# Kernel tuning notes

Hardware: AMD Instinct MI355X
Metric: run time of the kernel (lower is better)

The kernel has to match this reference:

```python
import jax, jax.numpy as jnp
import numpy as np

N = 100000   # nodes
E = 1200000  # edges
D = 64       # feature / hidden dim (heads=1)
L = 3        # num_layers
G = 64       # num graphs
SCALE = 1.0 / np.sqrt(D)


def setup_inputs() -> dict:
    key = jax.random.key(0)
    ks = jax.random.split(key, 12)
    inp = {
        "x": jax.random.normal(ks[0], (N, D), dtype=jnp.float32),
        "edge_index": jax.random.randint(ks[1], (2, E), 0, N, dtype=jnp.int64),
        "batch": jnp.sort(jax.random.randint(ks[2], (N,), 0, G, dtype=jnp.int64)),
        "Wq": jax.random.normal(ks[3], (L, D, D), dtype=jnp.float32) * 0.1,
        "bq": jax.random.normal(ks[4], (L, D), dtype=jnp.float32) * 0.1,
        "Wk": jax.random.normal(ks[5], (L, D, D), dtype=jnp.float32) * 0.1,
        "bk": jax.random.normal(ks[6], (L, D), dtype=jnp.float32) * 0.1,
        "Wv": jax.random.normal(ks[7], (L, D, D), dtype=jnp.float32) * 0.1,
        "bv": jax.random.normal(ks[8], (L, D), dtype=jnp.float32) * 0.1,
        "Ws": jax.random.normal(ks[9], (L, D, D), dtype=jnp.float32) * 0.1,
        "bs": jax.random.normal(ks[10], (L, D), dtype=jnp.float32) * 0.1,
    }
    return inp


def _transformer_conv(x, src, dst, Wq, bq, Wk, bk, Wv, bv, Ws, bs):
    # PyG TransformerConv, heads=1, concat=True, root_weight=True, beta=False
    q = x @ Wq + bq            # [N, D] query of target nodes
    k = x @ Wk + bk            # [N, D] key of source nodes
    v = x @ Wv + bv            # [N, D] value of source nodes
    logits = jnp.sum(q[dst] * k[src], axis=-1) * SCALE  # [E]
    # segment softmax over incoming edges of each target node
    m = jax.ops.segment_max(logits, dst, num_segments=N)        # [N]
    e = jnp.exp(logits - m[dst])                                 # [E]
    denom = jax.ops.segment_sum(e, dst, num_segments=N)         # [N]
    alpha = e / denom[dst]                                       # [E]
    agg = jax.ops.segment_sum(alpha[:, None] * v[src], dst, num_segments=N)  # [N, D]
    return agg + x @ Ws + bs   # root/skip connection


def reference(x, edge_index, batch, Wq, bq, Wk, bk, Wv, bv, Ws, bs):
    src, dst = edge_index[0], edge_index[1]
    for l in range(L):
        x = _transformer_conv(x, src, dst, Wq[l], bq[l], Wk[l], bk[l],
                              Wv[l], bv[l], Ws[l], bs[l])
        x = jax.nn.relu(x)
    # global_mean_pool
    sums = jax.ops.segment_sum(x, batch, num_segments=G)                  # [G, D]
    counts = jax.ops.segment_sum(jnp.ones((N,), x.dtype), batch, num_segments=G)
    graph_emb = sums / jnp.maximum(counts, 1.0)[:, None]
    return (x, graph_emb)
```

## Files before the change

kernel.cpp:

```cpp
#include <hip/hip_runtime.h>
#include <math.h>

#define DD 64

typedef _Float16 h2 __attribute__((ext_vector_type(2)));
typedef _Float16 h4 __attribute__((ext_vector_type(4)));
typedef _Float16 h8 __attribute__((ext_vector_type(8)));
typedef float f32x4 __attribute__((ext_vector_type(4)));

__global__ __launch_bounds__(64) void k_wconv(
    const float* __restrict__ Wq, const float* __restrict__ Wk,
    const float* __restrict__ Wv, const float* __restrict__ Ws,
    _Float16* __restrict__ wf)
{
  int bid = blockIdx.x;
  int layer = bid >> 5;
  int c = (bid >> 1) & 15;
  int s = bid & 1;
  int lane = threadIdx.x;
  int col = c * 16 + (lane & 15);
  int mi = col >> 6;
  const float* W = (mi == 0 ? Wq : mi == 1 ? Wk : mi == 2 ? Wv : Ws)
                   + (size_t)layer * DD * DD;
  int colw = col & 63;
  _Float16* o = wf + ((((size_t)(layer * 16 + c)) * 2 + s) * 64 + lane) * 8;
  #pragma unroll
  for (int j = 0; j < 8; ++j) {
    int k = s * 32 + (lane >> 4) * 8 + j;
    o[j] = (_Float16)W[k * DD + colw];
  }
}

__global__ __launch_bounds__(256) void k_xconv(
    const float* __restrict__ x, _Float16* __restrict__ xb, int total8)
{
  int i = blockIdx.x * 256 + threadIdx.x;
  if (i >= total8) return;
  float4 a = ((const float4*)x)[i * 2];
  float4 b = ((const float4*)x)[i * 2 + 1];
  h8 o;
  o[0] = (_Float16)a.x; o[1] = (_Float16)a.y; o[2] = (_Float16)a.z; o[3] = (_Float16)a.w;
  o[4] = (_Float16)b.x; o[5] = (_Float16)b.y; o[6] = (_Float16)b.z; o[7] = (_Float16)b.w;
  *(h8*)(xb + (size_t)i * 8) = o;
}

#define LH_STRIDE 200
#define LF_STRIDE 68
#define WAVE_LDS  (16 * 400 + 16 * 272)

__global__ __launch_bounds__(256) void k_projM(
    const _Float16* __restrict__ xb, const _Float16* __restrict__ wf,
    const float* __restrict__ bq, const float* __restrict__ bk,
    const float* __restrict__ bv, const float* __restrict__ bs,
    _Float16* __restrict__ qh, _Float16* __restrict__ kvh,
    float* __restrict__ sout, int n)
{
  __shared__ __align__(16) char lds[4 * WAVE_LDS];
  int wave = threadIdx.x >> 6;
  int lane = threadIdx.x & 63;
  int nbase = blockIdx.x * 64 + wave * 16;
  if (nbase >= n) return;

  char* wbase = lds + wave * WAVE_LDS;
  _Float16* lh = (_Float16*)wbase;
  float*    lf = (float*)(wbase + 16 * 400);

  const int cl = lane & 15;
  const int rq = lane >> 4;

  int ar = min(nbase + cl, n - 1);
  h8 a0 = *(const h8*)(xb + (size_t)ar * DD + rq * 8);
  h8 a1 = *(const h8*)(xb + (size_t)ar * DD + 32 + rq * 8);

  #pragma unroll
  for (int c = 0; c < 16; ++c) {
    const float* bp = (c < 4) ? bq : (c < 8) ? bk : (c < 12) ? bv : bs;
    const int fb = c * 16 + rq * 4;
    float4 b4 = *(const float4*)(bp + (fb & 63));
    f32x4 acc; acc[0] = b4.x; acc[1] = b4.y; acc[2] = b4.z; acc[3] = b4.w;
    const _Float16* wp = wf + ((size_t)(c * 2) * 64 + lane) * 8;
    h8 w0 = *(const h8*)(wp);
    h8 w1 = *(const h8*)(wp + 64 * 8);
    acc = __builtin_amdgcn_mfma_f32_16x16x32_f16(w0, a0, acc, 0, 0, 0);
    acc = __builtin_amdgcn_mfma_f32_16x16x32_f16(w1, a1, acc, 0, 0, 0);

    if (c < 12) {
      h4 o; o[0] = (_Float16)acc[0]; o[1] = (_Float16)acc[1];
      o[2] = (_Float16)acc[2]; o[3] = (_Float16)acc[3];
      *(h4*)(lh + cl * LH_STRIDE + fb) = o;
    } else {
      *(f32x4*)(lf + cl * LF_STRIDE + (fb - 192)) = acc;
    }
  }

  #pragma unroll
  for (int i = 0; i < 2; ++i) {
    int chunk = i * 64 + lane;
    int nd = chunk >> 3, co = chunk & 7;
    h8 v = *(const h8*)(lh + nd * LH_STRIDE + co * 8);
    if (nbase + nd < n)
      *(h8*)(qh + (size_t)(nbase + nd) * DD + co * 8) = v;
  }
  #pragma unroll
  for (int i = 0; i < 4; ++i) {
    int chunk = i * 64 + lane;
    int nd = chunk >> 4, co = chunk & 15;
    h8 v = *(const h8*)(lh + nd * LH_STRIDE + 64 + co * 8);
    if (nbase + nd < n)
      *(h8*)(kvh + (size_t)(nbase + nd) * 128 + co * 8) = v;
  }
  #pragma unroll
  for (int i = 0; i < 4; ++i) {
    int chunk = i * 64 + lane;
    int nd = chunk >> 4, co = chunk & 15;
    f32x4 v = *(const f32x4*)(lf + nd * LF_STRIDE + co * 4);
    if (nbase + nd < n)
      *(f32x4*)(sout + (size_t)(nbase + nd) * DD + co * 4) = v;
  }
}

__global__ __launch_bounds__(256) void k_hist(
    const int* __restrict__ dst, int* __restrict__ deg,
    unsigned short* __restrict__ pos, int ecnt)
{
  int e = (blockIdx.x * 256 + threadIdx.x) * 4;
  if (e + 3 < ecnt) {
    int4 d = *(const int4*)(dst + e);
    pos[e]     = (unsigned short)atomicAdd(deg + d.x, 1);
    pos[e + 1] = (unsigned short)atomicAdd(deg + d.y, 1);
    pos[e + 2] = (unsigned short)atomicAdd(deg + d.z, 1);
    pos[e + 3] = (unsigned short)atomicAdd(deg + d.w, 1);
  } else {
    for (; e < ecnt; ++e)
      pos[e] = (unsigned short)atomicAdd(deg + dst[e], 1);
  }
}

__global__ __launch_bounds__(1024) void k_scan(
    const int* __restrict__ deg, int* __restrict__ rowptr, int n)
{
  __shared__ int wsum[16];
  int lane = threadIdx.x & 63;
  int wave = threadIdx.x >> 6;
  if (threadIdx.x == 0) rowptr[0] = 0;
  int carry = 0;
  for (int base = 0; base < n; base += 4096) {
    int i = base + threadIdx.x * 4;
    int4 d = make_int4(0, 0, 0, 0);
    if (i + 3 < n) d = *(const int4*)(deg + i);
    else {
      if (i     < n) d.x = deg[i];
      if (i + 1 < n) d.y = deg[i + 1];
      if (i + 2 < n) d.z = deg[i + 2];
    }
    int s1 = d.x, s2 = s1 + d.y, s3 = s2 + d.z, s4 = s3 + d.w;
    int s = s4;
    #pragma unroll
    for (int off = 1; off < 64; off <<= 1) {
      int t = __shfl_up(s, off);
      if (lane >= off) s += t;
    }
    if (lane == 63) wsum[wave] = s;
    __syncthreads();
    if (wave == 0) {
      int ws = (lane < 16) ? wsum[lane] : 0;
      #pragma unroll
      for (int off = 1; off < 16; off <<= 1) {
        int t = __shfl_up(ws, off);
        if (lane >= off) ws += t;
      }
      if (lane < 16) wsum[lane] = ws;
    }
    __syncthreads();
    int excl = carry + ((wave > 0) ? wsum[wave - 1] : 0) + s - s4;
    if (i     < n) rowptr[i + 1] = excl + s1;
    if (i + 1 < n) rowptr[i + 2] = excl + s2;
    if (i + 2 < n) rowptr[i + 3] = excl + s3;
    if (i + 3 < n) rowptr[i + 4] = excl + s4;
    carry += wsum[15];
    __syncthreads();
  }
}

__global__ __launch_bounds__(256) void k_fill(
    const int* __restrict__ src, const int* __restrict__ dst,
    const int* __restrict__ rowptr, const unsigned short* __restrict__ pos,
    int* __restrict__ adj, int ecnt)
{
  int e = (blockIdx.x * 256 + threadIdx.x) * 4;
  if (e + 3 < ecnt) {
    int4 d = *(const int4*)(dst + e);
    int4 s = *(const int4*)(src + e);
    ushort4 p = *(const ushort4*)(pos + e);
    adj[rowptr[d.x] + p.x] = s.x;
    adj[rowptr[d.y] + p.y] = s.y;
    adj[rowptr[d.z] + p.z] = s.z;
    adj[rowptr[d.w] + p.w] = s.w;
  } else {
    for (; e < ecnt; ++e)
      adj[rowptr[dst[e]] + pos[e]] = src[e];
  }
}

#define H2OF(v, i) __builtin_shufflevector((v), (v), 2*(i), 2*(i)+1)

template<bool LAST>
__global__ __launch_bounds__(256) void k_node(
    const _Float16* __restrict__ qh, const _Float16* __restrict__ kvh,
    const int* __restrict__ rowptr, const int* __restrict__ adj,
    const float* __restrict__ sskip, float* __restrict__ outp,
    _Float16* __restrict__ xbnext, int n)
{
  int node = (blockIdx.x * blockDim.x + threadIdx.x) >> 6;
  node = __builtin_amdgcn_readfirstlane(node);
  int lane = threadIdx.x & 63;
  if (node >= n) return;
  const int g = lane >> 3;
  const int t = lane & 7;

  const h8 q8 = *(const h8*)((const char*)qh + (((unsigned)node << 7) + (t << 4)));
  const h2 qp0 = H2OF(q8, 0), qp1 = H2OF(q8, 1), qp2 = H2OF(q8, 2), qp3 = H2OF(q8, 3);

  const int e0 = rowptr[node], e1 = rowptr[node + 1];
  float mg = -1e30f, den = 0.f;
  float agg[8] = {0.f, 0.f, 0.f, 0.f, 0.f, 0.f, 0.f, 0.f};

  const char* kvb = (const char*)kvh;
  h8 kP, vP;
  {
    int sP = adj[e0 + g];
    unsigned off = ((unsigned)sP << 8) + ((unsigned)t << 4);
    kP = *(const h8*)(kvb + off);
    vP = *(const h8*)(kvb + off + 128);
  }

  for (int base = e0; base < e1; base += 8) {
    const h8 kc = kP, vc = vP;
    const bool valid = (base + g < e1);
    const int nb2 = base + 8;
    if (nb2 < e1) {
      int s2 = adj[nb2 + g];
      unsigned off = ((unsigned)s2 << 8) + ((unsigned)t << 4);
      kP = *(const h8*)(kvb + off);
      vP = *(const h8*)(kvb + off + 128);
    }

#if __has_builtin(__builtin_amdgcn_fdot2)
    float p = __builtin_amdgcn_fdot2(qp0, H2OF(kc, 0), 0.f, false);
    p = __builtin_amdgcn_fdot2(qp1, H2OF(kc, 1), p, false);
    p = __builtin_amdgcn_fdot2(qp2, H2OF(kc, 2), p, false);
    p = __builtin_amdgcn_fdot2(qp3, H2OF(kc, 3), p, false);
#else
    h2 ph = qp0 * H2OF(kc, 0);
    ph = qp1 * H2OF(kc, 1) + ph;
    ph = qp2 * H2OF(kc, 2) + ph;
    ph = qp3 * H2OF(kc, 3) + ph;
    float p = (float)ph.x + (float)ph.y;
#endif
    p += __shfl_xor(p, 1);
    p += __shfl_xor(p, 2);
    p += __shfl_xor(p, 4);
    p *= 0.125f;

    if (valid && p > mg) {
      float c = __expf(mg - p);
      den *= c;
      #pragma unroll
      for (int j = 0; j < 8; ++j) agg[j] *= c;
      mg = p;
    }
    float w = valid ? __expf(p - mg) : 0.f;
    den += w;
    #pragma unroll
    for (int j = 0; j < 8; ++j)
      agg[j] = fmaf(w, (float)vc[j], agg[j]);
  }

  float M = mg;
  M = fmaxf(M, __shfl_xor(M, 8));
  M = fmaxf(M, __shfl_xor(M, 16));
  M = fmaxf(M, __shfl_xor(M, 32));
  float f = __expf(mg - M);
  den *= f;
  den += __shfl_xor(den, 8);
  den += __shfl_xor(den, 16);
  den += __shfl_xor(den, 32);
  #pragma unroll
  for (int j = 0; j < 8; ++j) {
    agg[j] *= f;
    agg[j] += __shfl_xor(agg[j], 8);
    agg[j] += __shfl_xor(agg[j], 16);
    agg[j] += __shfl_xor(agg[j], 32);
  }

  if (g == 0) {
    float inv = (den > 0.f) ? (1.0f / den) : 0.f;
    const float* sp = (const float*)((const char*)sskip +
                      (((unsigned)node << 8) + (t << 5)));
    float4 sa = *(const float4*)(sp);
    float4 sb = *(const float4*)(sp + 4);
    float r[8];
    r[0] = fmaxf(fmaf(agg[0], inv, sa.x), 0.f);
    r[1] = fmaxf(fmaf(agg[1], inv, sa.y), 0.f);
    r[2] = fmaxf(fmaf(agg[2], inv, sa.z), 0.f);
    r[3] = fmaxf(fmaf(agg[3], inv, sa.w), 0.f);
    r[4] = fmaxf(fmaf(agg[4], inv, sb.x), 0.f);
    r[5] = fmaxf(fmaf(agg[5], inv, sb.y), 0.f);
    r[6] = fmaxf(fmaf(agg[6], inv, sb.z), 0.f);
    r[7] = fmaxf(fmaf(agg[7], inv, sb.w), 0.f);
    if (LAST) {
      float* op = (float*)((char*)outp + (((unsigned)node << 8) + (t << 5)));
      *(float4*)(op)     = make_float4(r[0], r[1], r[2], r[3]);
      *(float4*)(op + 4) = make_float4(r[4], r[5], r[6], r[7]);
    } else {
      h8 xh;
      #pragma unroll
      for (int j = 0; j < 8; ++j) xh[j] = (_Float16)r[j];
      *(h8*)((char*)xbnext + (((unsigned)node << 7) + (t << 4))) = xh;
    }
  }
}

__global__ __launch_bounds__(64) void k_pool_sum(
    const float* __restrict__ x, const int* __restrict__ batch,
    float* __restrict__ gsum, float* __restrict__ gcnt, int n)
{
  int lane = threadIdx.x;
  int n0 = blockIdx.x * 64;
  if (n0 >= n) return;
  int n1 = min(n0 + 64, n);
  float acc = 0.f;
  int g_prev = batch[n0];
  int run = 0;
  for (int nn = n0; nn < n1; ++nn) {
    int g = batch[nn];
    if (g != g_prev) {
      atomicAdd(gsum + (size_t)g_prev * DD + lane, acc);
      if (lane == 0) atomicAdd(gcnt + g_prev, (float)run);
      acc = 0.f; run = 0; g_prev = g;
    }
    acc += x[(size_t)nn * DD + lane];
    run++;
  }
  atomicAdd(gsum + (size_t)g_prev * DD + lane, acc);
  if (lane == 0) atomicAdd(gcnt + g_prev, (float)run);
}

__global__ __launch_bounds__(256) void k_pool_div(
    const float* __restrict__ gsum, const float* __restrict__ gcnt,
    float* __restrict__ emb, int gtot)
{
  int gid = blockIdx.x * blockDim.x + threadIdx.x;
  if (gid >= gtot * DD) return;
  int g = gid >> 6;
  emb[gid] = gsum[gid] / fmaxf(gcnt[g], 1.0f);
}

extern "C" void kernel_launch(void* const* d_in, const int* in_sizes, int n_in,
                              void* d_out, int out_size, void* d_ws, size_t ws_size,
                              hipStream_t stream)
{
  const float* x_in  = (const float*)d_in[0];
  const int*   ei    = (const int*)  d_in[1];
  const int*   batch = (const int*)  d_in[2];
  const float* Wq = (const float*)d_in[3];
  const float* bq = (const float*)d_in[4];
  const float* Wk = (const float*)d_in[5];
  const float* bk = (const float*)d_in[6];
  const float* Wv = (const float*)d_in[7];
  const float* bv = (const float*)d_in[8];
  const float* Ws = (const float*)d_in[9];
  const float* bs = (const float*)d_in[10];

  const int nd     = in_sizes[0];
  const int n      = nd / DD;
  const int ecnt   = in_sizes[1] / 2;
  const int layers = in_sizes[3] / (DD * DD);
  const int gtot   = (out_size - nd) / DD;

  const int* src = ei;
  const int* dst = ei + ecnt;

  char* cur = (char*)d_ws;
  float*     P0  = (float*)cur;     cur += (size_t)nd * 4;
  _Float16*  XB  = (_Float16*)cur;  cur += (size_t)nd * 2;
  _Float16*  QH  = (_Float16*)cur;  cur += (size_t)nd * 2;
  _Float16*  KVH = (_Float16*)cur;  cur += (size_t)nd * 4;
  _Float16*  WF  = (_Float16*)cur;  cur += (size_t)layers * 16384 * 2;
  int* rowptr = (int*)cur;          cur += (size_t)(n + 4) * 4;
  int* adj    = (int*)cur;          cur += (size_t)(ecnt + 8) * 4;
  int* deg    = (int*)cur;          cur += (size_t)n * 4;
  unsigned short* pos = (unsigned short*)cur; cur += (size_t)ecnt * 2;
  float* gsum = (float*)cur;        cur += (size_t)gtot * DD * 4;
  float* gcnt = (float*)cur;

  float* out = (float*)d_out;

  k_wconv<<<layers * 32, 64, 0, stream>>>(Wq, Wk, Wv, Ws, WF);
  k_xconv<<<(n * 8 + 255) / 256, 256, 0, stream>>>(x_in, XB, n * 8);
  hipMemsetAsync(adj + ecnt, 0, (size_t)(8 + n) * 4, stream);
  const int eb4 = (ecnt + 1023) / 1024;
  k_hist<<<eb4, 256, 0, stream>>>(dst, deg, pos, ecnt);
  k_scan<<<1, 1024, 0, stream>>>(deg, rowptr, n);
  k_fill<<<eb4, 256, 0, stream>>>(src, dst, rowptr, pos, adj, ecnt);

  const int pj = (n + 63) / 64;
  const int nb = (n * 64 + 255) / 256;

  for (int l = 0; l < layers; ++l) {
    const size_t bo = (size_t)l * DD;
    k_projM<<<pj, 256, 0, stream>>>(XB, WF + (size_t)l * 16384,
                                    bq + bo, bk + bo, bv + bo, bs + bo,
                                    QH, KVH, P0, n);
    if (l == layers - 1)
      k_node<true><<<nb, 256, 0, stream>>>(QH, KVH, rowptr, adj, P0, out, XB, n);
    else
      k_node<false><<<nb, 256, 0, stream>>>(QH, KVH, rowptr, adj, P0, out, XB, n);
  }

  hipMemsetAsync(gsum, 0, (size_t)(gtot * DD + gtot) * 4, stream);
  const int pbk = (n + 63) / 64;
  k_pool_sum<<<pbk, 64, 0, stream>>>(out, batch, gsum, gcnt, n);
  const int fb = (gtot * DD + 255) / 256;
  k_pool_div<<<fb, 256, 0, stream>>>(gsum, gcnt, out + (size_t)nd, gtot);
}
```

Measured before the change: 385.2 us.

## Map one node per 8-lane group with degree-sorted node order and parallel scan

Changes the attention kernel from one wavefront per node (8 edges in parallel) to eight nodes per wavefront, each handled by an 8-lane group that walks its edges sequentially. Nodes are bucketed by in-degree so the groups in a wavefront have similar loop trip counts, which limits divergence. The single-block prefix scan is replaced by a multi-block three-phase scan that also builds the degree histogram and the node order. This removes the cross-group softmax merge shuffles and wasted lanes for low-degree nodes (average degree is about 12). The cost is a serial per-edge dependency chain within each group and scattered node accesses in permuted order.

After: 350.7 us. -8.9%, faster.

```diff
diff --git a/kernel.cpp b/kernel.cpp
--- a/kernel.cpp
+++ b/kernel.cpp
@@ -136,50 +136,120 @@
   }
 }
 
-__global__ __launch_bounds__(1024) void k_scan(
-    const int* __restrict__ deg, int* __restrict__ rowptr, int n)
+__global__ __launch_bounds__(1024) void k_scanA(
+    const int* __restrict__ deg, int* __restrict__ rowptr,
+    int* __restrict__ btot, int* __restrict__ dbins, int n)
 {
   __shared__ int wsum[16];
-  int lane = threadIdx.x & 63;
-  int wave = threadIdx.x >> 6;
-  if (threadIdx.x == 0) rowptr[0] = 0;
-  int carry = 0;
-  for (int base = 0; base < n; base += 4096) {
-    int i = base + threadIdx.x * 4;
-    int4 d = make_int4(0, 0, 0, 0);
-    if (i + 3 < n) d = *(const int4*)(deg + i);
-    else {
-      if (i     < n) d.x = deg[i];
-      if (i + 1 < n) d.y = deg[i + 1];
-      if (i + 2 < n) d.z = deg[i + 2];
-    }
-    int s1 = d.x, s2 = s1 + d.y, s3 = s2 + d.z, s4 = s3 + d.w;
-    int s = s4;
+  __shared__ int lbin[256];
+  int tid = threadIdx.x;
+  int lane = tid & 63, wave = tid >> 6;
+  if (tid < 256) lbin[tid] = 0;
+  __syncthreads();
+  int i = blockIdx.x * 4096 + tid * 4;
+  int4 d = make_int4(0, 0, 0, 0);
+  if (i + 3 < n) d = *(const int4*)(deg + i);
+  else {
+    if (i     < n) d.x = deg[i];
+    if (i + 1 < n) d.y = deg[i + 1];
+    if (i + 2 < n) d.z = deg[i + 2];
+  }
+  if (i     < n) atomicAdd(&lbin[min(d.x, 255)], 1);
+  if (i + 1 < n) atomicAdd(&lbin[min(d.y, 255)], 1);
+  if (i + 2 < n) atomicAdd(&lbin[min(d.z, 255)], 1);
+  if (i + 3 < n) atomicAdd(&lbin[min(d.w, 255)], 1);
+
+  int s1 = d.x, s2 = s1 + d.y, s3 = s2 + d.z, s4 = s3 + d.w;
+  int s = s4;
+  #pragma unroll
+  for (int off = 1; off < 64; off <<= 1) {
+    int t = __shfl_up(s, off);
+    if (lane >= off) s += t;
+  }
+  if (lane == 63) wsum[wave] = s;
+  __syncthreads();
+  if (wave == 0) {
+    int ws = (lane < 16) ? wsum[lane] : 0;
     #pragma unroll
-    for (int off = 1; off < 64; off <<= 1) {
-      int t = __shfl_up(s, off);
-      if (lane >= off) s += t;
-    }
-    if (lane == 63) wsum[wave] = s;
-    __syncthreads();
-    if (wave == 0) {
-      int ws = (lane < 16) ? wsum[lane] : 0;
-      #pragma unroll
-      for (int off = 1; off < 16; off <<= 1) {
-        int t = __shfl_up(ws, off);
-        if (lane >= off) ws += t;
-      }
-      if (lane < 16) wsum[lane] = ws;
-    }
-    __syncthreads();
-    int excl = carry + ((wave > 0) ? wsum[wave - 1] : 0) + s - s4;
-    if (i     < n) rowptr[i + 1] = excl + s1;
-    if (i + 1 < n) rowptr[i + 2] = excl + s2;
-    if (i + 2 < n) rowptr[i + 3] = excl + s3;
-    if (i + 3 < n) rowptr[i + 4] = excl + s4;
-    carry += wsum[15];
-    __syncthreads();
-  }
+    for (int off = 1; off < 16; off <<= 1) {
+      int t = __shfl_up(ws, off);
+      if (lane >= off) ws += t;
+    }
+    if (lane < 16) wsum[lane] = ws;
+  }
+  __syncthreads();
+  int excl = ((wave > 0) ? wsum[wave - 1] : 0) + s - s4;
+  if (i     < n) rowptr[i + 1] = excl + s1;
+  if (i + 1 < n) rowptr[i + 2] = excl + s2;
+  if (i + 2 < n) rowptr[i + 3] = excl + s3;
+  if (i + 3 < n) rowptr[i + 4] = excl + s4;
+  if (tid == 0) {
+    if (blockIdx.x == 0) rowptr[0] = 0;
+    btot[blockIdx.x] = wsum[15];
+  }
+  if (tid < 256 && lbin[tid]) atomicAdd(&dbins[tid], lbin[tid]);
+}
+
+__global__ __launch_bounds__(64) void k_scanB(
+    int* __restrict__ btot, int nb, const int* __restrict__ dbins,
+    int* __restrict__ dcur)
+{
+  int lane = threadIdx.x;
+  int v = (lane < nb) ? btot[lane] : 0;
+  int s = v;
+  #pragma unroll
+  for (int off = 1; off < 64; off <<= 1) {
+    int t = __shfl_up(s, off);
+    if (lane >= off) s += t;
+  }
+  if (lane < nb) btot[lane] = s - v;
+
+  int4 dv = *(const int4*)(dbins + lane * 4);
+  int t1 = dv.x, t2 = t1 + dv.y, t3 = t2 + dv.z, t4 = t3 + dv.w;
+  int ss = t4;
+  #pragma unroll
+  for (int off = 1; off < 64; off <<= 1) {
+    int t = __shfl_up(ss, off);
+    if (lane >= off) ss += t;
+  }
+  int ex = ss - t4;
+  dcur[lane * 4]     = ex;
+  dcur[lane * 4 + 1] = ex + t1;
+  dcur[lane * 4 + 2] = ex + t2;
+  dcur[lane * 4 + 3] = ex + t3;
+}
+
+__global__ __launch_bounds__(1024) void k_scanC(
+    int* __restrict__ rowptr, const int* __restrict__ btot, int n)
+{
+  int off = btot[blockIdx.x];
+  if (off == 0) return;
+  int i = blockIdx.x * 4096 + threadIdx.x * 4;
+  #pragma unroll
+  for (int k = 1; k <= 4; ++k)
+    if (i + k <= n) rowptr[i + k] += off;
+}
+
+__global__ __launch_bounds__(1024) void k_dfill(
+    const int* __restrict__ deg, int* __restrict__ dcur,
+    int* __restrict__ order, int n)
+{
+  __shared__ int lcnt[256];
+  __shared__ int lbase[256];
+  int tid = threadIdx.x;
+  if (tid < 256) lcnt[tid] = 0;
+  __syncthreads();
+  int i = blockIdx.x * 1024 + tid;
+  int b = 0, slot = 0;
+  bool ok = (i < n);
+  if (ok) {
+    b = min(deg[i], 255);
+    slot = atomicAdd(&lcnt[b], 1);
+  }
+  __syncthreads();
+  if (tid < 256 && lcnt[tid]) lbase[tid] = atomicAdd(&dcur[tid], lcnt[tid]);
+  __syncthreads();
+  if (ok) order[lbase[b] + slot] = i;
 }
 
 __global__ __launch_bounds__(256) void k_fill(
@@ -208,38 +278,47 @@
 __global__ __launch_bounds__(256) void k_node(
     const _Float16* __restrict__ qh, const _Float16* __restrict__ kvh,
     const int* __restrict__ rowptr, const int* __restrict__ adj,
+    const int* __restrict__ order,
     const float* __restrict__ sskip, float* __restrict__ outp,
     _Float16* __restrict__ xbnext, int n)
 {
-  int node = (blockIdx.x * blockDim.x + threadIdx.x) >> 6;
-  node = __builtin_amdgcn_readfirstlane(node);
+  int wid = (blockIdx.x * blockDim.x + threadIdx.x) >> 6;
   int lane = threadIdx.x & 63;
-  if (node >= n) return;
   const int g = lane >> 3;
   const int t = lane & 7;
 
-  const h8 q8 = *(const h8*)((const char*)qh + (((unsigned)node << 7) + (t << 4)));
+  int idx = wid * 8 + g;
+  bool nok = (idx < n);
+  int node = order[nok ? idx : (n - 1)];
+
+  const h8 q8 = *(const h8*)(qh + (size_t)node * DD + t * 8);
   const h2 qp0 = H2OF(q8, 0), qp1 = H2OF(q8, 1), qp2 = H2OF(q8, 2), qp3 = H2OF(q8, 3);
 
-  const int e0 = rowptr[node], e1 = rowptr[node + 1];
+  const int e0 = rowptr[node];
+  const int d  = nok ? (rowptr[node + 1] - e0) : 0;
+
+  int dm = d;
+  dm = max(dm, __shfl_xor(dm, 8));
+  dm = max(dm, __shfl_xor(dm, 16));
+  dm = max(dm, __shfl_xor(dm, 32));
+
   float mg = -1e30f, den = 0.f;
   float agg[8] = {0.f, 0.f, 0.f, 0.f, 0.f, 0.f, 0.f, 0.f};
 
   const char* kvb = (const char*)kvh;
   h8 kP, vP;
-  {
-    int sP = adj[e0 + g];
-    unsigned off = ((unsigned)sP << 8) + ((unsigned)t << 4);
+  if (d > 0) {
+    int s = adj[e0];
+    unsigned off = ((unsigned)s << 8) + ((unsigned)t << 4);
     kP = *(const h8*)(kvb + off);
     vP = *(const h8*)(kvb + off + 128);
   }
 
-  for (int base = e0; base < e1; base += 8) {
+  for (int it = 0; it < dm; ++it) {
     const h8 kc = kP, vc = vP;
-    const bool valid = (base + g < e1);
-    const int nb2 = base + 8;
-    if (nb2 < e1) {
-      int s2 = adj[nb2 + g];
+    const bool valid = (it < d);
+    if (it + 1 < d) {
+      int s2 = adj[e0 + it + 1];
       unsigned off = ((unsigned)s2 << 8) + ((unsigned)t << 4);
       kP = *(const h8*)(kvb + off);
       vP = *(const h8*)(kvb + off + 128);
@@ -276,27 +355,9 @@
       agg[j] = fmaf(w, (float)vc[j], agg[j]);
   }
 
-  float M = mg;
-  M = fmaxf(M, __shfl_xor(M, 8));
-  M = fmaxf(M, __shfl_xor(M, 16));
-  M = fmaxf(M, __shfl_xor(M, 32));
-  float f = __expf(mg - M);
-  den *= f;
-  den += __shfl_xor(den, 8);
-  den += __shfl_xor(den, 16);
-  den += __shfl_xor(den, 32);
-  #pragma unroll
-  for (int j = 0; j < 8; ++j) {
-    agg[j] *= f;
-    agg[j] += __shfl_xor(agg[j], 8);
-    agg[j] += __shfl_xor(agg[j], 16);
-    agg[j] += __shfl_xor(agg[j], 32);
-  }
-
-  if (g == 0) {
+  if (nok) {
     float inv = (den > 0.f) ? (1.0f / den) : 0.f;
-    const float* sp = (const float*)((const char*)sskip +
-                      (((unsigned)node << 8) + (t << 5)));
+    const float* sp = sskip + (size_t)node * DD + t * 8;
     float4 sa = *(const float4*)(sp);
     float4 sb = *(const float4*)(sp + 4);
     float r[8];
@@ -309,14 +370,14 @@
     r[6] = fmaxf(fmaf(agg[6], inv, sb.z), 0.f);
     r[7] = fmaxf(fmaf(agg[7], inv, sb.w), 0.f);
     if (LAST) {
-      float* op = (float*)((char*)outp + (((unsigned)node << 8) + (t << 5)));
+      float* op = outp + (size_t)node * DD + t * 8;
       *(float4*)(op)     = make_float4(r[0], r[1], r[2], r[3]);
       *(float4*)(op + 4) = make_float4(r[4], r[5], r[6], r[7]);
     } else {
       h8 xh;
       #pragma unroll
       for (int j = 0; j < 8; ++j) xh[j] = (_Float16)r[j];
-      *(h8*)((char*)xbnext + (((unsigned)node << 7) + (t << 4))) = xh;
+      *(h8*)(xbnext + (size_t)node * DD + t * 8) = xh;
     }
   }
 }
@@ -390,6 +451,10 @@
   int* rowptr = (int*)cur;          cur += (size_t)(n + 4) * 4;
   int* adj    = (int*)cur;          cur += (size_t)(ecnt + 8) * 4;
   int* deg    = (int*)cur;          cur += (size_t)n * 4;
+  int* dbins  = (int*)cur;          cur += 256 * 4;
+  int* dcur   = (int*)cur;          cur += 256 * 4;
+  int* btot   = (int*)cur;          cur += 64 * 4;
+  int* order  = (int*)cur;          cur += (size_t)n * 4;
   unsigned short* pos = (unsigned short*)cur; cur += (size_t)ecnt * 2;
   float* gsum = (float*)cur;        cur += (size_t)gtot * DD * 4;
   float* gcnt = (float*)cur;
@@ -398,14 +463,18 @@
 
   k_wconv<<<layers * 32, 64, 0, stream>>>(Wq, Wk, Wv, Ws, WF);
   k_xconv<<<(n * 8 + 255) / 256, 256, 0, stream>>>(x_in, XB, n * 8);
-  hipMemsetAsync(adj + ecnt, 0, (size_t)(8 + n) * 4, stream);
+  hipMemsetAsync(deg, 0, (size_t)(n + 256) * 4, stream);
   const int eb4 = (ecnt + 1023) / 1024;
   k_hist<<<eb4, 256, 0, stream>>>(dst, deg, pos, ecnt);
-  k_scan<<<1, 1024, 0, stream>>>(deg, rowptr, n);
+  const int nbk = (n + 4095) / 4096;
+  k_scanA<<<nbk, 1024, 0, stream>>>(deg, rowptr, btot, dbins, n);
+  k_scanB<<<1, 64, 0, stream>>>(btot, nbk, dbins, dcur);
+  k_scanC<<<nbk, 1024, 0, stream>>>(rowptr, btot, n);
+  k_dfill<<<(n + 1023) / 1024, 1024, 0, stream>>>(deg, dcur, order, n);
   k_fill<<<eb4, 256, 0, stream>>>(src, dst, rowptr, pos, adj, ecnt);
 
   const int pj = (n + 63) / 64;
-  const int nb = (n * 64 + 255) / 256;
+  const int nb = (n + 31) / 32;
 
   for (int l = 0; l < layers; ++l) {
     const size_t bo = (size_t)l * DD;
@@ -413,9 +482,11 @@
                                     bq + bo, bk + bo, bv + bo, bs + bo,
                                     QH, KVH, P0, n);
     if (l == layers - 1)
-      k_node<true><<<nb, 256, 0, stream>>>(QH, KVH, rowptr, adj, P0, out, XB, n);
+      k_node<true><<<nb, 256, 0, stream>>>(QH, KVH, rowptr, adj, order,
+                                           P0, out, XB, n);
     else
-      k_node<false><<<nb, 256, 0, stream>>>(QH, KVH, rowptr, adj, P0, out, XB, n);
+      k_node<false><<<nb, 256, 0, stream>>>(QH, KVH, rowptr, adj, order,
+                                            P0, out, XB, n);
   }
 
   hipMemsetAsync(gsum, 0, (size_t)(gtot * DD + gtot) * 4, stream);
```
